# Kernel optimization log

Hardware: AMD Instinct MI355X
Metric: run time of the kernel (lower is better)

The kernel has to match this reference:

```python
import jax, jax.numpy as jnp
import numpy as np

B, T, C, HS = 8, 2048, 1024, 128

def setup_inputs() -> dict:
    key = jax.random.key(0)
    kx, kq, kk, kv = jax.random.split(key, 4)
    x = jax.random.normal(kx, (B, T, C), dtype=jnp.float32)
    # torch Linear(C, HS, bias=False): y = x @ W^T with W [HS, C].
    # We store the transposed form [C, HS] and right-multiply (same math).
    scale = 1.0 / np.sqrt(C)  # torch default init scale-ish; exact init irrelevant for correctness
    Wq = jax.random.normal(kq, (C, HS), dtype=jnp.float32) * scale
    Wk = jax.random.normal(kk, (C, HS), dtype=jnp.float32) * scale
    Wv = jax.random.normal(kv, (C, HS), dtype=jnp.float32) * scale
    return {"x": x, "Wq": Wq, "Wk": Wk, "Wv": Wv}

def reference(x, Wq, Wk, Wv):
    Bx, Tx, Cx = x.shape
    q = x @ Wq  # [B, T, HS]
    k = x @ Wk
    v = x @ Wv
    # NOTE: original scales by C**-0.5 where C = n_embd (not head_size)
    wei = jnp.einsum('btd,bsd->bts', q, k) * (Cx ** -0.5)  # [B, T, T]
    causal = jnp.tril(jnp.ones((Tx, Tx), dtype=bool))
    wei = jnp.where(causal, wei, -jnp.inf)
    wei = jax.nn.softmax(wei, axis=-1)
    # dropout rate 0.0 (eval semantics) -> identity
    return jnp.einsum('bts,bsd->btd', wei, v)  # [B, T, HS]
```

## Files before the change

### kernel.cpp

```cpp
#include <hip/hip_runtime.h>
#include <hip/hip_bf16.h>
#include <stdint.h>

typedef float f32x4 __attribute__((ext_vector_type(4)));
typedef float f32x4v __attribute__((ext_vector_type(4)));
typedef short short8 __attribute__((ext_vector_type(8)));
typedef unsigned short u16;
typedef unsigned short u16x8 __attribute__((ext_vector_type(8)));
typedef unsigned short u16x4 __attribute__((ext_vector_type(4)));

#define MFMA16x16x32 __builtin_amdgcn_mfma_f32_16x16x32_bf16

__device__ __forceinline__ u16 f2bf(float f) {
    unsigned int u = __builtin_bit_cast(unsigned int, f);
    u += 0x7fffu + ((u >> 16) & 1u);
    return (u16)(u >> 16);
}
__device__ __forceinline__ float bf2f(u16 v) {
    unsigned int u = ((unsigned int)v) << 16;
    return __builtin_bit_cast(float, u);
}

__device__ __forceinline__ void gload_lds16(const void* g, void* l) {
    __builtin_amdgcn_global_load_lds(
        (const __attribute__((address_space(1))) uint32_t*)g,
        (__attribute__((address_space(3))) uint32_t*)l, 16, 0, 0);
}

__device__ __forceinline__ int z_small(int na) {
    int za = (8 * na + 32) / 33;
    return za < 1 ? 1 : za;
}

__global__ void k_transpose_wf(const float* __restrict__ Wq, const float* __restrict__ Wk,
                               const float* __restrict__ Wv, u16* __restrict__ WTf) {
    int tid  = blockIdx.x * 256 + threadIdx.x;
    int f    = tid >> 6;
    int lane = tid & 63;
    int kt  = f / 48;
    int rem = f % 48;
    int ks  = rem / 24;
    int nc  = rem % 24;
    int col = nc * 16 + (lane & 15);
    int w   = col >> 7, n = col & 127;
    int k0  = kt * 64 + ks * 32 + (lane >> 4) * 8;
    const float* W = (w == 0) ? Wq : ((w == 1) ? Wk : Wv);
    u16x8 v;
#pragma unroll
    for (int j = 0; j < 8; ++j)
        v[j] = f2bf(W[(size_t)(k0 + j) * 128 + n]);
    *(u16x8*)(&WTf[(size_t)tid * 8]) = v;
}

__global__ __launch_bounds__(512) void k_qkv_gemm8(
    const float* __restrict__ x, const u16* __restrict__ WTf,
    u16* __restrict__ qb, u16* __restrict__ kb, u16* __restrict__ vT)
{
    __shared__ u16 abuf[2][64 * 64];
    __shared__ u16 bbuf[2][384 * 64];
    const int tid  = threadIdx.x;
    const int lane = tid & 63, wid = tid >> 6;
    const int wr = wid >> 2, wc = wid & 3;
    const int lrow = lane & 15, lk = lane >> 4;
    const int m0 = blockIdx.x * 64;

    const int arow = tid >> 3;
    const int aseg = tid & 7;
    const float* xsrc = x + (size_t)(m0 + arow) * 1024 + aseg * 8;

    f32x4 acc[2][6];
#pragma unroll
    for (int i = 0; i < 2; ++i)
#pragma unroll
        for (int j = 0; j < 6; ++j) acc[i][j] = (f32x4){0.f, 0.f, 0.f, 0.f};

#define LOADA(s0, s1, ktv)                                                     \
    s0 = *(const f32x4v*)(xsrc + (ktv) * 64);                                  \
    s1 = *(const f32x4v*)(xsrc + (ktv) * 64 + 4);

#define STOREA(buf, s0, s1)                                                    \
    {   u16x8 v;                                                               \
        v[0]=f2bf(s0[0]); v[1]=f2bf(s0[1]); v[2]=f2bf(s0[2]); v[3]=f2bf(s0[3]); \
        v[4]=f2bf(s1[0]); v[5]=f2bf(s1[1]); v[6]=f2bf(s1[2]); v[7]=f2bf(s1[3]); \
        *(u16x8*)(&buf[arow * 64 + ((aseg ^ (arow & 7)) << 3)]) = v; }

#define ISSUEB(buf, ktv)                                                       \
    {   const u16* bsrc = WTf + (size_t)(ktv) * 24576;                         \
        _Pragma("unroll") for (int i = 0; i < 6; ++i) {                        \
            int c = tid + i * 512;                                             \
            gload_lds16(bsrc + c * 8, &buf[c * 8]);                            \
        } }

#define COMPUTE(ab, bb)                                                        \
    _Pragma("unroll") for (int ks = 0; ks < 2; ++ks) {                         \
        short8 af[2];                                                          \
        _Pragma("unroll") for (int mf = 0; mf < 2; ++mf) {                     \
            int row = wr * 32 + mf * 16 + lrow;                                \
            int blk = (ks * 4 + lk) ^ (row & 7);                               \
            af[mf] = *(const short8*)(&ab[row * 64 + (blk << 3)]);             \
        }                                                                      \
        _Pragma("unroll") for (int nf = 0; nf < 6; ++nf) {                     \
            short8 bfr = *(const short8*)(&bb[(ks * 24 + wc * 6 + nf) * 512 + lane * 8]); \
            _Pragma("unroll") for (int mf = 0; mf < 2; ++mf)                   \
                acc[mf][nf] = MFMA16x16x32(af[mf], bfr, acc[mf][nf], 0, 0, 0); \
        } }

#define WAITBAR()                                                              \
    asm volatile("s_waitcnt vmcnt(2) lgkmcnt(0)\n\ts_barrier" ::: "memory");   \
    __builtin_amdgcn_sched_barrier(0);

    f32x4v a0A, a1A, a0B, a1B;
    LOADA(a0A, a1A, 0);
    LOADA(a0B, a1B, 1);
    STOREA(abuf[0], a0A, a1A);
    ISSUEB(bbuf[0], 0);
    LOADA(a0A, a1A, 2);
    WAITBAR();

    for (int kt = 0; kt < 16; kt += 2) {
        {
            const int ktn = (kt + 1 < 16) ? kt + 1 : 15;
            ISSUEB(bbuf[1], ktn);
            __builtin_amdgcn_sched_barrier(0);
            COMPUTE(abuf[0], bbuf[0]);
            STOREA(abuf[1], a0B, a1B);
            const int kp = (kt + 3 < 16) ? kt + 3 : 15;
            LOADA(a0B, a1B, kp);
            WAITBAR();
        }
        {
            const int ktn = (kt + 2 < 16) ? kt + 2 : 15;
            ISSUEB(bbuf[0], ktn);
            __builtin_amdgcn_sched_barrier(0);
            COMPUTE(abuf[1], bbuf[1]);
            STOREA(abuf[0], a0A, a1A);
            const int kp = (kt + 4 < 16) ? kt + 4 : 15;
            LOADA(a0A, a1A, kp);
            WAITBAR();
        }
    }
#undef LOADA
#undef STOREA
#undef ISSUEB
#undef COMPUTE
#undef WAITBAR

#pragma unroll
    for (int nf = 0; nf < 6; ++nf) {
        const int gc   = wc * 96 + nf * 16 + lrow;
        const int wsel = gc >> 7;
        const int col  = gc & 127;
#pragma unroll
        for (int mf = 0; mf < 2; ++mf) {
            const int row0 = m0 + wr * 32 + mf * 16 + lk * 4;
            if (wsel == 0) {
#pragma unroll
                for (int jj = 0; jj < 4; ++jj)
                    qb[(size_t)(row0 + jj) * 128 + col] = f2bf(acc[mf][nf][jj]);
            } else if (wsel == 1) {
#pragma unroll
                for (int jj = 0; jj < 4; ++jj)
                    kb[(size_t)(row0 + jj) * 128 + col] = f2bf(acc[mf][nf][jj]);
            } else {
                const int bb = row0 >> 11, t0 = row0 & 2047;
                u16x4 v;
#pragma unroll
                for (int jj = 0; jj < 4; ++jj) v[jj] = f2bf(acc[mf][nf][jj]);
                *(u16x4*)(&vT[((size_t)bb * 128 + col) * 2048 + t0]) = v;
            }
        }
    }
}

__global__ __launch_bounds__(256) void k_flash7(
    const u16* __restrict__ qb, const u16* __restrict__ kb, const u16* __restrict__ vT,
    u16* __restrict__ po, float* __restrict__ pm, float* __restrict__ pl)
{
    __shared__ u16 k_lds[2][64 * 128];
    __shared__ u16 v_lds[2][128 * 64];
    __shared__ u16 p_lds[4 * 16 * 64];
    const int tid  = threadIdx.x;
    const int lane = tid & 63, wid = tid >> 6;
    const int lrow = lane & 15, lk = lane >> 4;
    const int bx = blockIdx.x;
    const int b  = bx & 7;
    const int p  = (bx >> 3) & 15;
    const int z  = bx >> 7;

    const int na = p + 1;
    const int za = z_small(na);
    int qt, n, k, Z;
    if (z < za) { qt = p;      n = na;     k = z;      Z = za;     }
    else        { qt = 31 - p; n = 32 - p; k = z - za; Z = 8 - za; }
    const int t0 = (k * n) / Z;
    const int t1 = ((k + 1) * n) / Z;

    const int qrow0 = qt * 64;
    short8 qf[4];
    {
        const u16* qp = qb + ((size_t)b * 2048 + qrow0 + wid * 16 + lrow) * 128;
#pragma unroll
        for (int ks = 0; ks < 4; ++ks) qf[ks] = *(const short8*)(qp + ks * 32 + lk * 8);
    }
    f32x4 of[8];
#pragma unroll
    for (int i = 0; i < 8; ++i) of[i] = (f32x4){0.f, 0.f, 0.f, 0.f};
    float mrun[4], lsum[4];
#pragma unroll
    for (int j = 0; j < 4; ++j) { mrun[j] = -1e30f; lsum[j] = 0.f; }

    const u16* kbase = kb + (size_t)b * 2048 * 128;
    const u16* vbase = vT + (size_t)b * 128 * 2048;
    u16* pw = p_lds + wid * (16 * 64);

#define ISSUE_KV(c_, t_)                                                       \
    {   const int kv0_ = (t_) << 6;                                            \
        _Pragma("unroll") for (int i = 0; i < 4; ++i) {                        \
            int ch = tid + i * 256;                                            \
            int row = ch >> 4, blk = ch & 15;                                  \
            gload_lds16(kbase + (size_t)(kv0_ + row) * 128 + ((blk ^ (row & 7)) << 3), \
                        &k_lds[c_][ch * 8]);                                   \
        }                                                                      \
        _Pragma("unroll") for (int i = 0; i < 4; ++i) {                        \
            int ch = tid + i * 256;                                            \
            int row = ch >> 3, blk = ch & 7;                                   \
            gload_lds16(vbase + (size_t)row * 2048 + kv0_ + ((blk ^ (row & 7)) << 3), \
                        &v_lds[c_][ch * 8]);                                   \
        }                                                                      \
        __builtin_amdgcn_sched_barrier(0); }

    ISSUE_KV(0, t0);
    int c = 0;

    for (int t = t0; t < t1; ++t) {
        asm volatile("s_waitcnt vmcnt(0) lgkmcnt(0)\n\ts_barrier" ::: "memory");
        __builtin_amdgcn_sched_barrier(0);
        if (t + 1 < t1) ISSUE_KV(c ^ 1, t + 1);

        f32x4 sf[4];
#pragma unroll
        for (int nf = 0; nf < 4; ++nf) sf[nf] = (f32x4){0.f, 0.f, 0.f, 0.f};
#pragma unroll
        for (int ks = 0; ks < 4; ++ks)
#pragma unroll
            for (int nf = 0; nf < 4; ++nf) {
                int row = nf * 16 + lrow;
                int blk = (ks * 4 + lk) ^ (row & 7);
                short8 bfr = *(const short8*)(&k_lds[c][row * 128 + (blk << 3)]);
                sf[nf] = MFMA16x16x32(qf[ks], bfr, sf[nf], 0, 0, 0);
            }

        const bool diag = (t == n - 1);
#pragma unroll
        for (int nf = 0; nf < 4; ++nf)
#pragma unroll
            for (int jj = 0; jj < 4; ++jj) {
                float s = sf[nf][jj] * 0.03125f;
                if (diag && (nf * 16 + lrow > wid * 16 + lk * 4 + jj)) s = -1e30f;
                sf[nf][jj] = s;
            }
        float mt[4];
#pragma unroll
        for (int jj = 0; jj < 4; ++jj)
            mt[jj] = fmaxf(fmaxf(sf[0][jj], sf[1][jj]), fmaxf(sf[2][jj], sf[3][jj]));
#pragma unroll
        for (int off = 1; off < 16; off <<= 1)
#pragma unroll
            for (int jj = 0; jj < 4; ++jj)
                mt[jj] = fmaxf(mt[jj], __shfl_xor(mt[jj], off));
        bool small = true;
#pragma unroll
        for (int jj = 0; jj < 4; ++jj) small = small && (mt[jj] <= mrun[jj] + 8.f);
        if (!__all(small)) {
#pragma unroll
            for (int jj = 0; jj < 4; ++jj) {
                float mnew = fmaxf(mrun[jj], mt[jj]);
                float sc   = __expf(mrun[jj] - mnew);
                mrun[jj]   = mnew;
                lsum[jj]  *= sc;
#pragma unroll
                for (int df = 0; df < 8; ++df) of[df][jj] *= sc;
            }
        }
        float rs[4] = {0.f, 0.f, 0.f, 0.f};
#pragma unroll
        for (int nf = 0; nf < 4; ++nf)
#pragma unroll
            for (int jj = 0; jj < 4; ++jj) {
                float e = __expf(sf[nf][jj] - mrun[jj]);
                sf[nf][jj] = e;
                rs[jj] += e;
            }
#pragma unroll
        for (int off = 1; off < 16; off <<= 1)
#pragma unroll
            for (int jj = 0; jj < 4; ++jj)
                rs[jj] += __shfl_xor(rs[jj], off);
#pragma unroll
        for (int jj = 0; jj < 4; ++jj) lsum[jj] += rs[jj];

#pragma unroll
        for (int nf = 0; nf < 4; ++nf)
#pragma unroll
            for (int jj = 0; jj < 4; ++jj) {
                int row = lk * 4 + jj;
                int col = nf * 16 + lrow;
                pw[row * 64 + (((col >> 3) ^ (row & 7)) << 3) + (col & 7)] = f2bf(sf[nf][jj]);
            }
        asm volatile("s_waitcnt lgkmcnt(0)" ::: "memory");
        __builtin_amdgcn_sched_barrier(0);
        short8 paf[2];
#pragma unroll
        for (int ks2 = 0; ks2 < 2; ++ks2) {
            int blk = (ks2 * 4 + lk) ^ (lrow & 7);
            paf[ks2] = *(const short8*)(&pw[lrow * 64 + (blk << 3)]);
        }
#pragma unroll
        for (int ks2 = 0; ks2 < 2; ++ks2)
#pragma unroll
            for (int df = 0; df < 8; ++df) {
                int row = df * 16 + lrow;
                int blk = (ks2 * 4 + lk) ^ (row & 7);
                short8 vf = *(const short8*)(&v_lds[c][row * 64 + (blk << 3)]);
                of[df] = MFMA16x16x32(paf[ks2], vf, of[df], 0, 0, 0);
            }
        c ^= 1;
    }
#undef ISSUE_KV

    u16* poslab = po + (size_t)bx * (64 * 128);
#pragma unroll
    for (int df = 0; df < 8; ++df)
#pragma unroll
        for (int jj = 0; jj < 4; ++jj)
            poslab[(size_t)(wid * 16 + lk * 4 + jj) * 128 + df * 16 + lrow] = f2bf(of[df][jj]);
    if (lrow == 0) {
#pragma unroll
        for (int jj = 0; jj < 4; ++jj) {
            pm[(size_t)bx * 64 + wid * 16 + lk * 4 + jj] = mrun[jj];
            pl[(size_t)bx * 64 + wid * 16 + lk * 4 + jj] = lsum[jj];
        }
    }
}

__global__ __launch_bounds__(256) void k_combine(
    const u16* __restrict__ po, const float* __restrict__ pm, const float* __restrict__ pl,
    float* __restrict__ out)
{
    const int row  = blockIdx.x * 4 + (threadIdx.x >> 6);
    const int lane = threadIdx.x & 63;
    const int b  = row >> 11;
    const int t  = row & 2047;
    const int qt = t >> 6;
    const int r  = t & 63;

    const int p  = (qt < 16) ? qt : 31 - qt;
    const int za = z_small(p + 1);
    const int zlo = (qt < 16) ? 0 : za;
    const int zhi = (qt < 16) ? za : 8;

    float M = -1e30f;
    for (int z = zlo; z < zhi; ++z)
        M = fmaxf(M, pm[(size_t)(b + 8 * p + 128 * z) * 64 + r]);
    float den = 0.f, a0 = 0.f, a1 = 0.f;
    for (int z = zlo; z < zhi; ++z) {
        const int bxp = b + 8 * p + 128 * z;
        const float w = __expf(pm[(size_t)bxp * 64 + r] - M);
        den += w * pl[(size_t)bxp * 64 + r];
        const u16* slab = po + ((size_t)bxp * 64 + r) * 128;
        a0 += w * bf2f(slab[lane]);
        a1 += w * bf2f(slab[lane + 64]);
    }
    const float inv = 1.f / den;
    out[(size_t)row * 128 + lane]      = a0 * inv;
    out[(size_t)row * 128 + lane + 64] = a1 * inv;
}

extern "C" void kernel_launch(void* const* d_in, const int* in_sizes, int n_in,
                              void* d_out, int out_size, void* d_ws, size_t ws_size,
                              hipStream_t stream) {
    const float* x  = (const float*)d_in[0];
    const float* Wq = (const float*)d_in[1];
    const float* Wk = (const float*)d_in[2];
    const float* Wv = (const float*)d_in[3];
    float* out = (float*)d_out;

    char* ws = (char*)d_ws;
    u16*   qb  = (u16*)(ws);
    u16*   kb  = (u16*)(ws + (size_t)4  * 1048576);
    u16*   vT  = (u16*)(ws + (size_t)8  * 1048576);
    u16*   WTf = (u16*)(ws + (size_t)12 * 1048576);
    u16*   po  = (u16*)(ws + (size_t)13 * 1048576);
    float* pm  = (float*)(ws + (size_t)47 * 1048576);
    float* pl  = (float*)(ws + (size_t)48 * 1048576);

    k_transpose_wf<<<192, 256, 0, stream>>>(Wq, Wk, Wv, WTf);
    k_qkv_gemm8<<<256, 512, 0, stream>>>(x, WTf, qb, kb, vT);
    k_flash7<<<1024, 256, 0, stream>>>(qb, kb, vT, po, pm, pl);
    k_combine<<<4096, 256, 0, stream>>>(po, pm, pl, out);
}
```

Measured before the change: 75.51 us.

## Enlarge flash attention query tile to 128 rows with 8 waves per block

The flash kernel now processes 128 query rows per block using 512 threads (8 waves), so each K/V tile loaded into LDS is reused by twice as many query rows. Block count halves, and the split-KV partitioning and the combine kernel indexing are reworked for the 128-row tiles. Masking moves from a single diagonal-tile check to a per-wave condition on key position, because a 128-row tile now spans two 64-key diagonal tiles. This cuts K/V global-to-LDS traffic per query row at the cost of fewer blocks (less parallelism), more LDS per block, and coarser work balancing.

```diff
diff --git a/kernel.cpp b/kernel.cpp
--- a/kernel.cpp
+++ b/kernel.cpp
@@ -27,9 +27,10 @@
         (__attribute__((address_space(3))) uint32_t*)l, 16, 0, 0);
 }
 
-__device__ __forceinline__ int z_small(int na) {
-    int za = (8 * na + 32) / 33;
-    return za < 1 ? 1 : za;
+__device__ __forceinline__ int z_small2(int na) {
+    int za = (8 * na + 33) / 34;
+    za = za < 1 ? 1 : za;
+    return za > 7 ? 7 : za;
 }
 
 __global__ void k_transpose_wf(const float* __restrict__ Wq, const float* __restrict__ Wk,
@@ -172,33 +173,33 @@
     }
 }
 
-__global__ __launch_bounds__(256) void k_flash7(
+__global__ __launch_bounds__(512) void k_flash8(
     const u16* __restrict__ qb, const u16* __restrict__ kb, const u16* __restrict__ vT,
     u16* __restrict__ po, float* __restrict__ pm, float* __restrict__ pl)
 {
     __shared__ u16 k_lds[2][64 * 128];
     __shared__ u16 v_lds[2][128 * 64];
-    __shared__ u16 p_lds[4 * 16 * 64];
+    __shared__ u16 p_lds[8 * 16 * 64];
     const int tid  = threadIdx.x;
     const int lane = tid & 63, wid = tid >> 6;
     const int lrow = lane & 15, lk = lane >> 4;
     const int bx = blockIdx.x;
     const int b  = bx & 7;
-    const int p  = (bx >> 3) & 15;
-    const int z  = bx >> 7;
-
-    const int na = p + 1;
-    const int za = z_small(na);
-    int qt, n, k, Z;
-    if (z < za) { qt = p;      n = na;     k = z;      Z = za;     }
-    else        { qt = 31 - p; n = 32 - p; k = z - za; Z = 8 - za; }
-    const int t0 = (k * n) / Z;
-    const int t1 = ((k + 1) * n) / Z;
-
-    const int qrow0 = qt * 64;
+    const int pu = (bx >> 3) & 7;
+    const int z  = bx >> 6;
+
+    const int na = 2 * pu + 2;
+    const int za = z_small2(na);
+    int qt2, n2, k, Z;
+    if (z < za) { qt2 = pu;      n2 = na;          k = z;      Z = za;     }
+    else        { qt2 = 15 - pu; n2 = 32 - 2 * pu; k = z - za; Z = 8 - za; }
+    const int t0 = (k * n2) / Z;
+    const int t1 = ((k + 1) * n2) / Z;
+
+    const int qbase = qt2 * 128 + wid * 16;
     short8 qf[4];
     {
-        const u16* qp = qb + ((size_t)b * 2048 + qrow0 + wid * 16 + lrow) * 128;
+        const u16* qp = qb + ((size_t)b * 2048 + qbase + lrow) * 128;
 #pragma unroll
         for (int ks = 0; ks < 4; ++ks) qf[ks] = *(const short8*)(qp + ks * 32 + lk * 8);
     }
@@ -215,14 +216,14 @@
 
 #define ISSUE_KV(c_, t_)                                                       \
     {   const int kv0_ = (t_) << 6;                                            \
-        _Pragma("unroll") for (int i = 0; i < 4; ++i) {                        \
-            int ch = tid + i * 256;                                            \
+        _Pragma("unroll") for (int i = 0; i < 2; ++i) {                        \
+            int ch = tid + i * 512;                                            \
             int row = ch >> 4, blk = ch & 15;                                  \
             gload_lds16(kbase + (size_t)(kv0_ + row) * 128 + ((blk ^ (row & 7)) << 3), \
                         &k_lds[c_][ch * 8]);                                   \
         }                                                                      \
-        _Pragma("unroll") for (int i = 0; i < 4; ++i) {                        \
-            int ch = tid + i * 256;                                            \
+        _Pragma("unroll") for (int i = 0; i < 2; ++i) {                        \
+            int ch = tid + i * 512;                                            \
             int row = ch >> 3, blk = ch & 7;                                   \
             gload_lds16(vbase + (size_t)row * 2048 + kv0_ + ((blk ^ (row & 7)) << 3), \
                         &v_lds[c_][ch * 8]);                                   \
@@ -233,6 +234,7 @@
     int c = 0;
 
     for (int t = t0; t < t1; ++t) {
+        const int kv0 = t << 6;
         asm volatile("s_waitcnt vmcnt(0) lgkmcnt(0)\n\ts_barrier" ::: "memory");
         __builtin_amdgcn_sched_barrier(0);
         if (t + 1 < t1) ISSUE_KV(c ^ 1, t + 1);
@@ -250,13 +252,13 @@
                 sf[nf] = MFMA16x16x32(qf[ks], bfr, sf[nf], 0, 0, 0);
             }
 
-        const bool diag = (t == n - 1);
+        const bool needmask = (kv0 + 63 > qbase);
 #pragma unroll
         for (int nf = 0; nf < 4; ++nf)
 #pragma unroll
             for (int jj = 0; jj < 4; ++jj) {
                 float s = sf[nf][jj] * 0.03125f;
-                if (diag && (nf * 16 + lrow > wid * 16 + lk * 4 + jj)) s = -1e30f;
+                if (needmask && (kv0 + nf * 16 + lrow > qbase + lk * 4 + jj)) s = -1e30f;
                 sf[nf][jj] = s;
             }
         float mt[4];
@@ -328,7 +330,7 @@
     }
 #undef ISSUE_KV
 
-    u16* poslab = po + (size_t)bx * (64 * 128);
+    u16* poslab = po + (size_t)bx * (128 * 128);
 #pragma unroll
     for (int df = 0; df < 8; ++df)
 #pragma unroll
@@ -337,8 +339,8 @@
     if (lrow == 0) {
 #pragma unroll
         for (int jj = 0; jj < 4; ++jj) {
-            pm[(size_t)bx * 64 + wid * 16 + lk * 4 + jj] = mrun[jj];
-            pl[(size_t)bx * 64 + wid * 16 + lk * 4 + jj] = lsum[jj];
+            pm[(size_t)bx * 128 + wid * 16 + lk * 4 + jj] = mrun[jj];
+            pl[(size_t)bx * 128 + wid * 16 + lk * 4 + jj] = lsum[jj];
         }
     }
 }
@@ -349,25 +351,25 @@
 {
     const int row  = blockIdx.x * 4 + (threadIdx.x >> 6);
     const int lane = threadIdx.x & 63;
-    const int b  = row >> 11;
-    const int t  = row & 2047;
-    const int qt = t >> 6;
-    const int r  = t & 63;
-
-    const int p  = (qt < 16) ? qt : 31 - qt;
-    const int za = z_small(p + 1);
-    const int zlo = (qt < 16) ? 0 : za;
-    const int zhi = (qt < 16) ? za : 8;
+    const int b   = row >> 11;
+    const int t   = row & 2047;
+    const int qt2 = t >> 7;
+    const int r   = t & 127;
+
+    const int p2 = (qt2 < 8) ? qt2 : 15 - qt2;
+    const int za = z_small2(2 * p2 + 2);
+    const int zlo = (qt2 < 8) ? 0 : za;
+    const int zhi = (qt2 < 8) ? za : 8;
 
     float M = -1e30f;
     for (int z = zlo; z < zhi; ++z)
-        M = fmaxf(M, pm[(size_t)(b + 8 * p + 128 * z) * 64 + r]);
+        M = fmaxf(M, pm[(size_t)(b + 8 * p2 + 64 * z) * 128 + r]);
     float den = 0.f, a0 = 0.f, a1 = 0.f;
     for (int z = zlo; z < zhi; ++z) {
-        const int bxp = b + 8 * p + 128 * z;
-        const float w = __expf(pm[(size_t)bxp * 64 + r] - M);
-        den += w * pl[(size_t)bxp * 64 + r];
-        const u16* slab = po + ((size_t)bxp * 64 + r) * 128;
+        const int bxp = b + 8 * p2 + 64 * z;
+        const float w = __expf(pm[(size_t)bxp * 128 + r] - M);
+        den += w * pl[(size_t)bxp * 128 + r];
+        const u16* slab = po + ((size_t)bxp * 128 + r) * 128;
         a0 += w * bf2f(slab[lane]);
         a1 += w * bf2f(slab[lane + 64]);
     }
@@ -396,6 +398,6 @@
 
     k_transpose_wf<<<192, 256, 0, stream>>>(Wq, Wk, Wv, WTf);
     k_qkv_gemm8<<<256, 512, 0, stream>>>(x, WTf, qb, kb, vT);
-    k_flash7<<<1024, 256, 0, stream>>>(qb, kb, vT, po, pm, pl);
+    k_flash8<<<512, 512, 0, stream>>>(qb, kb, vT, po, pm, pl);
     k_combine<<<4096, 256, 0, stream>>>(po, pm, pl, out);
 }
```

New measurement: 76.31 us. Within noise of the previous version (+1.1%).
